# Kernel optimization log

Hardware: AMD Instinct MI355X
Metric: run time of the kernel (lower is better)

Reference implementation:

```python
import jax, jax.numpy as jnp
import numpy as np

B, Li, Lo, C, E, H = 256, 512, 128, 16, 128, 256


def setup_inputs() -> dict:
    key = jax.random.key(0)
    ks = jax.random.split(key, 12)
    s = 0.08  # small init scale to keep LSTM gates in a sane range
    return {
        "inputs": jax.random.normal(ks[0], (B, Li, C), jnp.float32),
        "emb_W": jax.random.normal(ks[1], (E, C), jnp.float32) * s,
        "emb_b": jnp.zeros((E,), jnp.float32),
        "enc_Wih": jax.random.normal(ks[2], (4 * H, E), jnp.float32) * s,
        "enc_Whh": jax.random.normal(ks[3], (4 * H, H), jnp.float32) * s,
        "enc_b": jnp.zeros((4 * H,), jnp.float32),  # b_ih + b_hh fused
        "dec_Wih": jax.random.normal(ks[4], (4 * H, E), jnp.float32) * s,
        "dec_Whh": jax.random.normal(ks[5], (4 * H, H), jnp.float32) * s,
        "dec_b": jnp.zeros((4 * H,), jnp.float32),
        "att_W1": jax.random.normal(ks[6], (H, H), jnp.float32) * s,
        "att_W2": jax.random.normal(ks[7], (H, H), jnp.float32) * s,  # n_layers*H = H
        "att_V": jax.random.normal(ks[8], (1, H), jnp.float32) * s,
        "dec_input0": jax.random.uniform(ks[9], (E,), jnp.float32),
    }


def _lstm_cell(x, h, c, Wih, Whh, b):
    # PyTorch gate order: i, f, g, o
    g = x @ Wih.T + h @ Whh.T + b
    i, f, gg, o = jnp.split(g, 4, axis=-1)
    c = jax.nn.sigmoid(f) * c + jax.nn.sigmoid(i) * jnp.tanh(gg)
    h = jax.nn.sigmoid(o) * jnp.tanh(c)
    return h, c


def reference(inputs, emb_W, emb_b, enc_Wih, enc_Whh, enc_b,
              dec_Wih, dec_Whh, dec_b, att_W1, att_W2, att_V, dec_input0):
    Bq = inputs.shape[0]
    emb = inputs @ emb_W.T + emb_b  # [B, Li, E]

    # ---- Encoder LSTM over Li (single layer, unidirectional) ----
    h0 = jnp.zeros((Bq, H), inputs.dtype)
    c0 = jnp.zeros((Bq, H), inputs.dtype)

    def enc_step(carry, x_t):
        h, c = carry
        h, c = _lstm_cell(x_t, h, c, enc_Wih, enc_Whh, enc_b)
        return (h, c), h

    (h_enc, c_enc), enc_hs = jax.lax.scan(enc_step, (h0, c0), emb.transpose(1, 0, 2))
    enc_hiddens = enc_hs.transpose(1, 0, 2)  # [B, Li, H]

    # Precompute W1 @ encoder_hiddens once (same math as per-step W1(enc))
    enc_proj = enc_hiddens @ att_W1.T  # [B, Li, H]

    # ---- Decoder: Lo pointer steps ----
    def dec_step(carry, _):
        h, c, x = carry
        h, c = _lstm_cell(x, h, c, dec_Wih, dec_Whh, dec_b)
        dec_term = h @ att_W2.T  # [B, H]
        scores = jnp.tanh(enc_proj + dec_term[:, None, :]) @ att_V[0]  # [B, Li]
        idx = jnp.argmax(scores, axis=1)  # [B]
        x_next = jnp.take_along_axis(emb, idx[:, None, None], axis=1)[:, 0, :]  # [B, E]
        return (h, c, x_next), (scores, idx)

    x0 = jnp.broadcast_to(dec_input0, (Bq, E))
    _, (all_scores, pointers) = jax.lax.scan(
        dec_step, (h_enc, c_enc, x0), None, length=Lo)
    logits = all_scores.transpose(1, 2, 0)  # [B, Li, Lo]
    return logits, pointers.T  # pointers [B, Lo]
```

## Files before the change

### kernel.cpp

```cpp
#include <hip/hip_runtime.h>
#include <math.h>


typedef float vf4 __attribute__((ext_vector_type(4)));

__device__ __forceinline__ float dot4(vf4 a, vf4 b) {
  return a.x * b.x + a.y * b.y + a.z * b.z + a.w * b.w;
}

__device__ __forceinline__ float tanh_fast(float x) {
  float e = __expf(2.0f * x);
  return 1.0f - 2.0f * __builtin_amdgcn_rcpf(e + 1.0f);
}

__device__ __forceinline__ vf4 ld1_sc1(const vf4* p) {
  vf4 v;
  asm volatile("global_load_dwordx4 %0, %1, off sc0 sc1\n\ts_waitcnt vmcnt(0)"
               : "=v"(v) : "v"(p) : "memory");
  return v;
}

__device__ __forceinline__ void ld2_sc1(const vf4* p0, const vf4* p1, vf4& v0, vf4& v1) {
  asm volatile(
      "global_load_dwordx4 %0, %2, off sc0 sc1\n\t"
      "global_load_dwordx4 %1, %3, off sc0 sc1\n\t"
      "s_waitcnt vmcnt(0)"
      : "=&v"(v0), "=&v"(v1) : "v"(p0), "v"(p1) : "memory");
}

#define AL(p) __hip_atomic_load((p), __ATOMIC_RELAXED, __HIP_MEMORY_SCOPE_AGENT)
#define AS(p, v) __hip_atomic_store((p), (v), __ATOMIC_RELAXED, __HIP_MEMORY_SCOPE_AGENT)
#define DRAIN() asm volatile("s_waitcnt vmcnt(0)" ::: "memory")

__global__ __launch_bounds__(512, 2) void pointer_net_kernel(
    const float* __restrict__ inputs,
    const float* __restrict__ emb_W,
    const float* __restrict__ emb_b,
    const float* __restrict__ eWih,
    const float* __restrict__ eWhh,
    const float* __restrict__ eb,
    const float* __restrict__ dWih,
    const float* __restrict__ dWhh,
    const float* __restrict__ db,
    const float* __restrict__ W1,
    const float* __restrict__ W2,
    const float* __restrict__ Vv,
    const float* __restrict__ d0,
    float* __restrict__ out,
    float* __restrict__ encp,
    float* __restrict__ ring,
    int* __restrict__ hflags,
    unsigned int* __restrict__ pflags)
{
  __shared__ float lds_h[16 * 260];
  __shared__ float lds_part[256 * 68];
  __shared__ float lds_pw[256 * 17];
  __shared__ float lds_wx[2][1024];
  __shared__ float lds_sc[512];
  __shared__ float lds_de[512];

  const int tid = threadIdx.x;
  const int B = blockIdx.x;
  const int bi = ((B & 7) << 1) | (B >> 7);
  const int dj = (B >> 3) & 15;
  const int bl = tid >> 4, dl = tid & 15;
  const int b = (bi << 4) + bl;
  const int d = (dj << 4) + dl;
  const int b_own = (bi << 4) + dj;
  const int lane = tid & 63;
  const int wv = tid >> 6;
  const int sdl = tid & 15, sks = (tid >> 4) & 15;
  const int sb4 = (tid >> 8) << 2;
  const int sbh8 = (tid >> 8) << 3;

  int* fgA = hflags + (bi << 5);
  int* fgB = fgA + 16;
  unsigned int* pfg = pflags + (bi << 4);
  float* ring_g = ring + ((size_t)bi << 14);

  asm volatile("buffer_inv sc1\n\ts_waitcnt vmcnt(0)" ::: "memory");

  vf4 wreg[16], w1reg[4];
  {
    const int k0 = sks << 4;
#pragma unroll
    for (int g = 0; g < 4; ++g) {
      const float* wr = eWhh + ((size_t)((g << 8) + (dj << 4) + sdl)) * 256 + k0;
#pragma unroll
      for (int q = 0; q < 4; ++q) wreg[(g << 2) + q] = *(const vf4*)(wr + (q << 2));
    }
    const float* w1r = W1 + ((size_t)(dj << 4) + sdl) * 256 + k0;
#pragma unroll
    for (int q = 0; q < 4; ++q) w1reg[q] = *(const vf4*)(w1r + (q << 2));
  }

  for (int idx = tid; idx < 1024; idx += 512) {
    int c = idx >> 6, jj = idx & 63;
    int j = ((jj & 3) << 8) + (dj << 4) + (jj >> 2);
    float se = 0.f, sd = 0.f;
    const float* er = eWih + (size_t)j * 128;
    const float* dr = dWih + (size_t)j * 128;
    for (int e = 0; e < 128; ++e) {
      float ew = emb_W[(e << 4) + c];
      se += er[e] * ew;
      sd += dr[e] * ew;
    }
    lds_wx[0][idx] = se;
    lds_wx[1][idx] = sd;
  }
  float benr[4] = {0, 0, 0, 0}, dber[4] = {0, 0, 0, 0},
        dbemb[4] = {0, 0, 0, 0}, g0r[4] = {0, 0, 0, 0};
  if (tid < 256) {
    for (int g = 0; g < 4; ++g) {
      int j = (g << 8) + d;
      const float* er = eWih + (size_t)j * 128;
      const float* dr = dWih + (size_t)j * 128;
      float s1 = 0.f, s2 = 0.f, s3 = 0.f;
      for (int e = 0; e < 128; ++e) {
        s1 += er[e] * emb_b[e];
        s2 += dr[e] * emb_b[e];
        s3 += dr[e] * d0[e];
      }
      benr[g] = eb[j] + s1;
      dber[g] = db[j];
      dbemb[g] = s2;
      g0r[g] = s3;
    }
  }
  vf4 v4a = *((const vf4*)Vv + lane);
  float c_reg = 0.0f;
  __syncthreads();

#define POLL(fb, u)                                                              \
  if (tid < 64) {                                                                \
    const int* fp = (fb) + (tid & 15);                                           \
    for (;;) {                                                                   \
      int f;                                                                     \
      asm volatile("global_load_dword %0, %1, off sc0 sc1\n\ts_waitcnt vmcnt(0)" \
                   : "=v"(f) : "v"(fp) : "memory");                              \
      if (__ballot(f >= (u)) == ~0ull) break;                                    \
      __builtin_amdgcn_s_sleep(1);                                               \
    }                                                                            \
  }                                                                              \
  __syncthreads();

#define LOAD_HALF(slot, half)                                                    \
  {                                                                              \
    int grow = ((half) << 3) + (tid >> 6);                                       \
    int col = (tid & 63) << 2;                                                   \
    vf4 v = ld1_sc1((const vf4*)(ring_g + ((size_t)(slot) << 12) + (grow << 8) + col)); \
    *(vf4*)(lds_h + grow * 260 + col) = v;                                       \
  }                                                                              \
  __syncthreads();

#define LOAD_FULL(slot)                                                          \
  {                                                                              \
    int r0 = tid >> 6, col = (tid & 63) << 2;                                    \
    const float* base = ring_g + ((size_t)(slot) << 12);                         \
    vf4 v0, v1;                                                                  \
    ld2_sc1((const vf4*)(base + (r0 << 8) + col),                                \
            (const vf4*)(base + ((r0 + 8) << 8) + col), v0, v1);                 \
    *(vf4*)(lds_h + r0 * 260 + col) = v0;                                        \
    *(vf4*)(lds_h + (r0 + 8) * 260 + col) = v1;                                  \
  }                                                                              \
  __syncthreads();

#define SLICE_BODY(bb, do_g, do_w)                                               \
  {                                                                              \
    const float* hb = lds_h + (bb)*260 + (sks << 4);                             \
    vf4 h0 = *(const vf4*)(hb);                                                  \
    vf4 h1 = *(const vf4*)(hb + 4);                                              \
    vf4 h2 = *(const vf4*)(hb + 8);                                              \
    vf4 h3 = *(const vf4*)(hb + 12);                                             \
    int r = ((bb) << 4) + sks;                                                   \
    if (do_g) {                                                                  \
      vf4 s;                                                                     \
      s.x = dot4(h0, wreg[0]) + dot4(h1, wreg[1]) + dot4(h2, wreg[2]) +          \
            dot4(h3, wreg[3]);                                                   \
      s.y = dot4(h0, wreg[4]) + dot4(h1, wreg[5]) + dot4(h2, wreg[6]) +          \
            dot4(h3, wreg[7]);                                                   \
      s.z = dot4(h0, wreg[8]) + dot4(h1, wreg[9]) + dot4(h2, wreg[10]) +         \
            dot4(h3, wreg[11]);                                                  \
      s.w = dot4(h0, wreg[12]) + dot4(h1, wreg[13]) + dot4(h2, wreg[14]) +       \
            dot4(h3, wreg[15]);                                                  \
      *(vf4*)(lds_part + r * 68 + (sdl << 2)) = s;                               \
    }                                                                            \
    if (do_w) {                                                                  \
      lds_pw[r * 17 + sdl] = dot4(h0, w1reg[0]) + dot4(h1, w1reg[1]) +           \
                             dot4(h2, w1reg[2]) + dot4(h3, w1reg[3]);            \
    }                                                                            \
  }

#define SLICE_HALF(half, do_g, do_w)                                             \
  for (int q = 0; q < 4; ++q) SLICE_BODY(((half) << 3) + sb4 + q, do_g, do_w)

#define SLICE_FULL(do_g, do_w)                                                   \
  for (int q = 0; q < 8; ++q) SLICE_BODY(sbh8 + q, do_g, do_w)

#define RED_GATES(a0, a1, a2, a3)                                                \
  _Pragma("unroll") for (int ks = 0; ks < 16; ++ks) {                            \
    vf4 p = *(const vf4*)(lds_part + ((bl << 4) + ks) * 68 + (dl << 2));         \
    a0 += p.x; a1 += p.y; a2 += p.z; a3 += p.w;                                  \
  }

#define WX_ADD(sel, xp, a0, a1, a2, a3)                                          \
  for (int c = 0; c < 16; c += 4) {                                              \
    vf4 xv = *(const vf4*)((xp) + c);                                            \
    vf4 wx0 = *(const vf4*)(&lds_wx[sel][((c + 0) << 6) + (dl << 2)]);           \
    vf4 wx1 = *(const vf4*)(&lds_wx[sel][((c + 1) << 6) + (dl << 2)]);           \
    vf4 wx2 = *(const vf4*)(&lds_wx[sel][((c + 2) << 6) + (dl << 2)]);           \
    vf4 wx3 = *(const vf4*)(&lds_wx[sel][((c + 3) << 6) + (dl << 2)]);           \
    a0 += xv.x * wx0.x + xv.y * wx1.x + xv.z * wx2.x + xv.w * wx3.x;             \
    a1 += xv.x * wx0.y + xv.y * wx1.y + xv.z * wx2.y + xv.w * wx3.y;             \
    a2 += xv.x * wx0.z + xv.y * wx1.z + xv.z * wx2.z + xv.w * wx3.z;             \
    a3 += xv.x * wx0.w + xv.y * wx1.w + xv.z * wx2.w + xv.w * wx3.w;             \
  }

#define ACT_PUB(a0, a1, a2, a3, slot)                                            \
  {                                                                              \
    float ig = 1.0f / (1.0f + expf(-(a0)));                                      \
    float fg = 1.0f / (1.0f + expf(-(a1)));                                      \
    float gg = tanhf(a2);                                                        \
    float og = 1.0f / (1.0f + expf(-(a3)));                                      \
    c_reg = fg * c_reg + ig * gg;                                                \
    float hn = og * tanhf(c_reg);                                                \
    AS(ring_g + ((size_t)(slot) << 12) + (bl << 8) + d, hn);                     \
  }

  {
    if (tid < 256) {
      float a0 = benr[0], a1 = benr[1], a2 = benr[2], a3 = benr[3];
      const float* xp = inputs + (size_t)((b << 9) << 4);
      WX_ADD(0, xp, a0, a1, a2, a3);
      ACT_PUB(a0, a1, a2, a3, 1);
    }
    DRAIN();
    __syncthreads();
    if (tid == 0) { AS(fgA + dj, 1); AS(fgB + dj, 1); }
  }

  for (int t = 1; t < 512; ++t) {
    float ax0 = 0.f, ax1 = 0.f, ax2 = 0.f, ax3 = 0.f;
    if (tid < 256) {
      ax0 = benr[0]; ax1 = benr[1]; ax2 = benr[2]; ax3 = benr[3];
      const float* xp = inputs + (size_t)(((b << 9) + t) << 4);
      WX_ADD(0, xp, ax0, ax1, ax2, ax3);
    }

    POLL(fgA, t);
    if (t > 1 && tid >= 256 && tid < 384) {
      int tq = tid - 256;
      int blq = 8 + (tq >> 4);
      float ev = 0.f;
#pragma unroll
      for (int ks = 0; ks < 16; ++ks) ev += lds_pw[((blq << 4) + ks) * 17 + (tq & 15)];
      AS(encp + ((((size_t)((bi << 4) + blq)) << 9) + (t - 2) << 8) + d, ev);
    }
    LOAD_HALF(t & 3, 0);
    SLICE_HALF(0, 1, 0);
    __syncthreads();
    if (tid < 128) {
      RED_GATES(ax0, ax1, ax2, ax3);
      ACT_PUB(ax0, ax1, ax2, ax3, (t + 1) & 3);
    }
    DRAIN();
    __syncthreads();
    if (tid == 0) AS(fgA + dj, t + 1);
    SLICE_HALF(0, 0, 1);

    POLL(fgB, t);
    if (tid >= 256 && tid < 384) {
      int tq = tid - 256;
      int blq = tq >> 4;
      float ev = 0.f;
#pragma unroll
      for (int ks = 0; ks < 16; ++ks) ev += lds_pw[((blq << 4) + ks) * 17 + (tq & 15)];
      AS(encp + ((((size_t)((bi << 4) + blq)) << 9) + (t - 1) << 8) + d, ev);
    }
    LOAD_HALF(t & 3, 1);
    SLICE_HALF(1, 1, 0);
    __syncthreads();
    if (tid >= 128 && tid < 256) {
      RED_GATES(ax0, ax1, ax2, ax3);
      ACT_PUB(ax0, ax1, ax2, ax3, (t + 1) & 3);
    }
    DRAIN();
    __syncthreads();
    if (tid == 0) AS(fgB + dj, t + 1);
    SLICE_HALF(1, 0, 1);
  }

  POLL(fgA, 512);
  POLL(fgB, 512);
  if (tid >= 256 && tid < 384) {
    int tq = tid - 256;
    int blq = 8 + (tq >> 4);
    float ev = 0.f;
#pragma unroll
    for (int ks = 0; ks < 16; ++ks) ev += lds_pw[((blq << 4) + ks) * 17 + (tq & 15)];
    AS(encp + ((((size_t)((bi << 4) + blq)) << 9) + 510 << 8) + d, ev);
  }
  LOAD_FULL(0);
  SLICE_FULL(0, 1);
  __syncthreads();
  if (tid < 256) {
    float ev = 0.f;
#pragma unroll
    for (int ks = 0; ks < 16; ++ks) ev += lds_pw[((bl << 4) + ks) * 17 + dl];
    AS(encp + (((size_t)((b << 9) + 511)) << 8) + d, ev);
  }
  {
    const int k0 = sks << 4;
#pragma unroll
    for (int g = 0; g < 4; ++g) {
      const float* wr = dWhh + ((size_t)((g << 8) + (dj << 4) + sdl)) * 256 + k0;
#pragma unroll
      for (int q = 0; q < 4; ++q) wreg[(g << 2) + q] = *(const vf4*)(wr + (q << 2));
    }
  }
  SLICE_FULL(1, 0);
  __syncthreads();

  for (int j = 0; j < 128; ++j) {
    const int u = 513 + j;
    if (tid < 256) {
      float a0 = dber[0], a1 = dber[1], a2 = dber[2], a3 = dber[3];
      RED_GATES(a0, a1, a2, a3);
      if (j == 0) {
        a0 += g0r[0]; a1 += g0r[1]; a2 += g0r[2]; a3 += g0r[3];
      } else {
        a0 += dbemb[0]; a1 += dbemb[1]; a2 += dbemb[2]; a3 += dbemb[3];
        unsigned int pf;
        for (;;) {
          pf = AL(pfg + bl);
          if ((pf >> 16) == (unsigned int)(j - 1)) break;
          __builtin_amdgcn_s_sleep(1);
        }
        const float* xp = inputs + (size_t)(((b << 9) + (int)(pf & 0xffff)) << 4);
        WX_ADD(1, xp, a0, a1, a2, a3);
      }
      ACT_PUB(a0, a1, a2, a3, u & 3);
    }
    DRAIN();
    __syncthreads();
    if (tid == 0) AS(fgA + dj, u);

    POLL(fgA, u);
    LOAD_FULL(u & 3);

    const vf4* bse = (const vf4*)(encp + ((size_t)b_own << 17));
    vf4 A[8], Bv[8];
#pragma unroll
    for (int jj = 0; jj < 8; ++jj)
      A[jj] = bse[((size_t)(wv + (jj << 3)) << 6) + lane];

    {
      const int d2 = tid & 255, hf = tid >> 8;
      const float* hrow = lds_h + dj * 260 + (hf << 7);
      const float* w2r = W2 + (size_t)d2 * 256 + (hf << 7);
      float a = 0.f;
      for (int k = 0; k < 128; k += 4) {
        vf4 h4 = *(const vf4*)(hrow + k);
        vf4 q = *(const vf4*)(w2r + k);
        a += dot4(h4, q);
      }
      lds_de[(hf << 8) + d2] = a;
    }
    __syncthreads();

    {
      vf4 p0 = *((const vf4*)lds_de + lane);
      vf4 p1 = *((const vf4*)(lds_de + 256) + lane);
      vf4 d4; d4.x = p0.x + p1.x; d4.y = p0.y + p1.y;
              d4.z = p0.z + p1.z; d4.w = p0.w + p1.w;
      for (int ch = 0; ch < 8; ++ch) {
        if (ch < 7) {
#pragma unroll
          for (int jj = 0; jj < 8; ++jj)
            Bv[jj] = bse[((size_t)(wv + (((ch + 1) * 8 + jj) << 3)) << 6) + lane];
        }
#pragma unroll
        for (int jj = 0; jj < 8; ++jj) {
          int li = wv + (((ch << 3) + jj) << 3);
          vf4 e4 = A[jj];
          float s = v4a.x * tanh_fast(e4.x + d4.x)
                  + v4a.y * tanh_fast(e4.y + d4.y)
                  + v4a.z * tanh_fast(e4.z + d4.z)
                  + v4a.w * tanh_fast(e4.w + d4.w);
#pragma unroll
          for (int off = 32; off; off >>= 1) s += __shfl_down(s, off);
          if (lane == 0) lds_sc[li] = s;
        }
#pragma unroll
        for (int jj = 0; jj < 8; ++jj) A[jj] = Bv[jj];
      }
      __syncthreads();

      __builtin_nontemporal_store(lds_sc[tid],
          &out[(size_t)(((b_own << 9) + tid) << 7) + j]);

      if (tid < 64) {
        float bs = -3.402823466e38f;
        int bix = 0;
        for (int i = 0; i < 8; ++i) {
          int idx = (i << 6) + tid;
          float s = lds_sc[idx];
          if (s > bs || (s == bs && idx < bix)) { bs = s; bix = idx; }
        }
#pragma unroll
        for (int off = 32; off; off >>= 1) {
          float os = __shfl_down(bs, off);
          int oi = __shfl_down(bix, off);
          if (os > bs || (os == bs && oi < bix)) { bs = os; bix = oi; }
        }
        if (tid == 0) {
          AS(pfg + dj, ((unsigned int)j << 16) | (unsigned int)bix);
          __builtin_nontemporal_store((float)bix,
              &out[(size_t)16777216 + (b_own << 7) + j]);
        }
      }
    }

    if (j < 127) {
      SLICE_FULL(1, 0);
      __syncthreads();
    }
  }
#undef POLL
#undef LOAD_HALF
#undef LOAD_FULL
#undef SLICE_BODY
#undef SLICE_HALF
#undef SLICE_FULL
#undef RED_GATES
#undef WX_ADD
#undef ACT_PUB
}

extern "C" void kernel_launch(void* const* d_in, const int* in_sizes, int n_in,
                              void* d_out, int out_size, void* d_ws, size_t ws_size,
                              hipStream_t stream) {
  (void)in_sizes; (void)n_in; (void)out_size;
  const float* inputs = (const float*)d_in[0];
  const float* emb_W  = (const float*)d_in[1];
  const float* emb_b  = (const float*)d_in[2];
  const float* eWih   = (const float*)d_in[3];
  const float* eWhh   = (const float*)d_in[4];
  const float* eb     = (const float*)d_in[5];
  const float* dWih   = (const float*)d_in[6];
  const float* dWhh   = (const float*)d_in[7];
  const float* db     = (const float*)d_in[8];
  const float* W1     = (const float*)d_in[9];
  const float* W2     = (const float*)d_in[10];
  const float* Vv     = (const float*)d_in[11];
  const float* d0     = (const float*)d_in[12];

  float* out = (float*)d_out;
  float* encp   = (float*)d_ws;
  float* ring   = encp + 33554432;
  int*   hflags = (int*)(ring + 262144);
  unsigned int* pflags = (unsigned int*)(hflags + 512);

  size_t need = (size_t)(33554432 + 262144 + 768) * 4;
  if (ws_size < need) return;

  hipLaunchKernelGGL(pointer_net_kernel, dim3(256), dim3(512), 0, stream,
                     inputs, emb_W, emb_b, eWih, eWhh, eb, dWih, dWhh, db,
                     W1, W2, Vv, d0, out, encp, ring, hflags, pflags);
}
```

Baseline: 7.575 ms.

## Replace per-step flag barriers with data-embedded tag-bit polling on ring buffer

Removes the per-timestep flag publish/poll handshake between cooperating blocks. Each hidden value now carries a parity tag in its mantissa LSB, and consumers spin on the ring data itself until every element shows the expected tag. This cuts a store-drain plus flag round trip from the recurrent critical path. In exchange, one mantissa bit of h is lost and the handshake relies on ring initialization and epoch parity being correct.

Measured after the change: 7.113 ms. 1.06x faster.

```diff
diff --git a/kernel.cpp b/kernel.cpp
--- a/kernel.cpp
+++ b/kernel.cpp
@@ -30,7 +30,13 @@
 
 #define AL(p) __hip_atomic_load((p), __ATOMIC_RELAXED, __HIP_MEMORY_SCOPE_AGENT)
 #define AS(p, v) __hip_atomic_store((p), (v), __ATOMIC_RELAXED, __HIP_MEMORY_SCOPE_AGENT)
+#define ASU(p, v) __hip_atomic_store((unsigned*)(p), (unsigned)(v), __ATOMIC_RELAXED, __HIP_MEMORY_SCOPE_AGENT)
 #define DRAIN() asm volatile("s_waitcnt vmcnt(0)" ::: "memory")
+
+#define OK1(x, e) ((__float_as_uint(x) & 1u) == (unsigned)(e))
+
+#define INIT_SIG 0x5A17C0DE
+#define DONE_SIG 0x5A17D00E
 
 __global__ __launch_bounds__(512, 2) void pointer_net_kernel(
     const float* __restrict__ inputs,
@@ -80,6 +86,16 @@
 
   asm volatile("buffer_inv sc1\n\ts_waitcnt vmcnt(0)" ::: "memory");
 
+  if (tid < 256) {
+#pragma unroll
+    for (int s = 0; s < 4; ++s) {
+      ASU(ring_g + ((size_t)s << 12) + (bl << 8) + d, (s == 0) ? 0u : 1u);
+    }
+  }
+  DRAIN();
+  __syncthreads();
+  if (tid == 0) AS(fgA + dj, INIT_SIG);
+
   vf4 wreg[16], w1reg[4];
   {
     const int k0 = sks << 4;
@@ -131,37 +147,54 @@
   float c_reg = 0.0f;
   __syncthreads();
 
-#define POLL(fb, u)                                                              \
+#define POLLX(fb, sig)                                                           \
   if (tid < 64) {                                                                \
     const int* fp = (fb) + (tid & 15);                                           \
     for (;;) {                                                                   \
       int f;                                                                     \
       asm volatile("global_load_dword %0, %1, off sc0 sc1\n\ts_waitcnt vmcnt(0)" \
                    : "=v"(f) : "v"(fp) : "memory");                              \
-      if (__ballot(f >= (u)) == ~0ull) break;                                    \
+      if (__ballot(f == (sig)) == ~0ull) break;                                  \
+      __builtin_amdgcn_s_sleep(8);                                               \
+    }                                                                            \
+  }                                                                              \
+  __syncthreads();
+
+#define PLOAD_HALF(slot, half, e)                                                \
+  {                                                                              \
+    int grow = ((half) << 3) + wv;                                               \
+    int col = lane << 2;                                                         \
+    const vf4* tp = (const vf4*)(ring_g + ((size_t)(slot) << 12) + (grow << 8) + col); \
+    for (;;) {                                                                   \
+      vf4 v = ld1_sc1(tp);                                                       \
+      bool ok = OK1(v.x, e) && OK1(v.y, e) && OK1(v.z, e) && OK1(v.w, e);        \
+      if (__ballot(ok) == ~0ull) {                                               \
+        *(vf4*)(lds_h + grow * 260 + col) = v;                                   \
+        break;                                                                   \
+      }                                                                          \
       __builtin_amdgcn_s_sleep(1);                                               \
     }                                                                            \
   }                                                                              \
   __syncthreads();
 
-#define LOAD_HALF(slot, half)                                                    \
+#define PLOAD_FULL(slot, e)                                                      \
   {                                                                              \
-    int grow = ((half) << 3) + (tid >> 6);                                       \
-    int col = (tid & 63) << 2;                                                   \
-    vf4 v = ld1_sc1((const vf4*)(ring_g + ((size_t)(slot) << 12) + (grow << 8) + col)); \
-    *(vf4*)(lds_h + grow * 260 + col) = v;                                       \
-  }                                                                              \
-  __syncthreads();
-
-#define LOAD_FULL(slot)                                                          \
-  {                                                                              \
-    int r0 = tid >> 6, col = (tid & 63) << 2;                                    \
+    int r0 = wv, col = lane << 2;                                                \
     const float* base = ring_g + ((size_t)(slot) << 12);                         \
-    vf4 v0, v1;                                                                  \
-    ld2_sc1((const vf4*)(base + (r0 << 8) + col),                                \
-            (const vf4*)(base + ((r0 + 8) << 8) + col), v0, v1);                 \
-    *(vf4*)(lds_h + r0 * 260 + col) = v0;                                        \
-    *(vf4*)(lds_h + (r0 + 8) * 260 + col) = v1;                                  \
+    const vf4* p0 = (const vf4*)(base + (r0 << 8) + col);                        \
+    const vf4* p1 = (const vf4*)(base + ((r0 + 8) << 8) + col);                  \
+    for (;;) {                                                                   \
+      vf4 v0, v1;                                                                \
+      ld2_sc1(p0, p1, v0, v1);                                                   \
+      bool ok = OK1(v0.x, e) && OK1(v0.y, e) && OK1(v0.z, e) && OK1(v0.w, e) &&  \
+                OK1(v1.x, e) && OK1(v1.y, e) && OK1(v1.z, e) && OK1(v1.w, e);    \
+      if (__ballot(ok) == ~0ull) {                                               \
+        *(vf4*)(lds_h + r0 * 260 + col) = v0;                                    \
+        *(vf4*)(lds_h + (r0 + 8) * 260 + col) = v1;                              \
+        break;                                                                   \
+      }                                                                          \
+      __builtin_amdgcn_s_sleep(1);                                               \
+    }                                                                            \
   }                                                                              \
   __syncthreads();
 
@@ -216,7 +249,7 @@
     a3 += xv.x * wx0.w + xv.y * wx1.w + xv.z * wx2.w + xv.w * wx3.w;             \
   }
 
-#define ACT_PUB(a0, a1, a2, a3, slot)                                            \
+#define ACT_PUB(a0, a1, a2, a3, slot, tagbit)                                    \
   {                                                                              \
     float ig = 1.0f / (1.0f + expf(-(a0)));                                      \
     float fg = 1.0f / (1.0f + expf(-(a1)));                                      \
@@ -224,22 +257,22 @@
     float og = 1.0f / (1.0f + expf(-(a3)));                                      \
     c_reg = fg * c_reg + ig * gg;                                                \
     float hn = og * tanhf(c_reg);                                                \
-    AS(ring_g + ((size_t)(slot) << 12) + (bl << 8) + d, hn);                     \
-  }
-
-  {
-    if (tid < 256) {
-      float a0 = benr[0], a1 = benr[1], a2 = benr[2], a3 = benr[3];
-      const float* xp = inputs + (size_t)((b << 9) << 4);
-      WX_ADD(0, xp, a0, a1, a2, a3);
-      ACT_PUB(a0, a1, a2, a3, 1);
-    }
-    DRAIN();
-    __syncthreads();
-    if (tid == 0) { AS(fgA + dj, 1); AS(fgB + dj, 1); }
-  }
+    unsigned hu = (__float_as_uint(hn) & ~1u) | (unsigned)(tagbit);              \
+    ASU(ring_g + ((size_t)(slot) << 12) + (bl << 8) + d, hu);                    \
+  }
+
+  if (tid < 256) {
+    float a0 = benr[0], a1 = benr[1], a2 = benr[2], a3 = benr[3];
+    const float* xp = inputs + (size_t)((b << 9) << 4);
+    WX_ADD(0, xp, a0, a1, a2, a3);
+    ACT_PUB(a0, a1, a2, a3, 1, 0);
+  }
+
+  POLLX(fgA, INIT_SIG);
 
   for (int t = 1; t < 512; ++t) {
+    const int e = (t >> 2) & 1;
+    const int pt = ((t + 1) >> 2) & 1;
     float ax0 = 0.f, ax1 = 0.f, ax2 = 0.f, ax3 = 0.f;
     if (tid < 256) {
       ax0 = benr[0]; ax1 = benr[1]; ax2 = benr[2]; ax3 = benr[3];
@@ -247,7 +280,6 @@
       WX_ADD(0, xp, ax0, ax1, ax2, ax3);
     }
 
-    POLL(fgA, t);
     if (t > 1 && tid >= 256 && tid < 384) {
       int tq = tid - 256;
       int blq = 8 + (tq >> 4);
@@ -256,19 +288,16 @@
       for (int ks = 0; ks < 16; ++ks) ev += lds_pw[((blq << 4) + ks) * 17 + (tq & 15)];
       AS(encp + ((((size_t)((bi << 4) + blq)) << 9) + (t - 2) << 8) + d, ev);
     }
-    LOAD_HALF(t & 3, 0);
+    PLOAD_HALF(t & 3, 0, e);
     SLICE_HALF(0, 1, 0);
     __syncthreads();
     if (tid < 128) {
       RED_GATES(ax0, ax1, ax2, ax3);
-      ACT_PUB(ax0, ax1, ax2, ax3, (t + 1) & 3);
-    }
-    DRAIN();
+      ACT_PUB(ax0, ax1, ax2, ax3, (t + 1) & 3, pt);
+    }
+    SLICE_HALF(0, 0, 1);
     __syncthreads();
-    if (tid == 0) AS(fgA + dj, t + 1);
-    SLICE_HALF(0, 0, 1);
-
-    POLL(fgB, t);
+
     if (tid >= 256 && tid < 384) {
       int tq = tid - 256;
       int blq = tq >> 4;
@@ -277,21 +306,17 @@
       for (int ks = 0; ks < 16; ++ks) ev += lds_pw[((blq << 4) + ks) * 17 + (tq & 15)];
       AS(encp + ((((size_t)((bi << 4) + blq)) << 9) + (t - 1) << 8) + d, ev);
     }
-    LOAD_HALF(t & 3, 1);
+    PLOAD_HALF(t & 3, 1, e);
     SLICE_HALF(1, 1, 0);
     __syncthreads();
     if (tid >= 128 && tid < 256) {
       RED_GATES(ax0, ax1, ax2, ax3);
-      ACT_PUB(ax0, ax1, ax2, ax3, (t + 1) & 3);
-    }
-    DRAIN();
+      ACT_PUB(ax0, ax1, ax2, ax3, (t + 1) & 3, pt);
+    }
+    SLICE_HALF(1, 0, 1);
     __syncthreads();
-    if (tid == 0) AS(fgB + dj, t + 1);
-    SLICE_HALF(1, 0, 1);
-  }
-
-  POLL(fgA, 512);
-  POLL(fgB, 512);
+  }
+
   if (tid >= 256 && tid < 384) {
     int tq = tid - 256;
     int blq = 8 + (tq >> 4);
@@ -300,7 +325,7 @@
     for (int ks = 0; ks < 16; ++ks) ev += lds_pw[((blq << 4) + ks) * 17 + (tq & 15)];
     AS(encp + ((((size_t)((bi << 4) + blq)) << 9) + 510 << 8) + d, ev);
   }
-  LOAD_FULL(0);
+  PLOAD_FULL(0, 0);
   SLICE_FULL(0, 1);
   __syncthreads();
   if (tid < 256) {
@@ -319,10 +344,14 @@
     }
   }
   SLICE_FULL(1, 0);
-  __syncthreads();
+  DRAIN();
+  __syncthreads();
+  if (tid == 0) AS(fgB + dj, DONE_SIG);
+  POLLX(fgB, DONE_SIG);
 
   for (int j = 0; j < 128; ++j) {
     const int u = 513 + j;
+    const int eu = (u >> 2) & 1;
     if (tid < 256) {
       float a0 = dber[0], a1 = dber[1], a2 = dber[2], a3 = dber[3];
       RED_GATES(a0, a1, a2, a3);
@@ -339,14 +368,9 @@
         const float* xp = inputs + (size_t)(((b << 9) + (int)(pf & 0xffff)) << 4);
         WX_ADD(1, xp, a0, a1, a2, a3);
       }
-      ACT_PUB(a0, a1, a2, a3, u & 3);
-    }
-    DRAIN();
-    __syncthreads();
-    if (tid == 0) AS(fgA + dj, u);
-
-    POLL(fgA, u);
-    LOAD_FULL(u & 3);
+      ACT_PUB(a0, a1, a2, a3, u & 3, eu);
+    }
+    PLOAD_FULL(u & 3, eu);
 
     const vf4* bse = (const vf4*)(encp + ((size_t)b_own << 17));
     vf4 A[8], Bv[8];
@@ -426,9 +450,9 @@
       __syncthreads();
     }
   }
-#undef POLL
-#undef LOAD_HALF
-#undef LOAD_FULL
+#undef POLLX
+#undef PLOAD_HALF
+#undef PLOAD_FULL
 #undef SLICE_BODY
 #undef SLICE_HALF
 #undef SLICE_FULL
```
